# Kernel optimization log

Hardware: AMD Instinct MI355X
Metric: run time of the kernel (lower is better)

## Reference

```python
import jax, jax.numpy as jnp
import numpy as np

# alpha clamp limits: balance=False -> [exp(-1/5), exp(-1/25)]
ALPHA_MIN = float(np.exp(-1.0 / 5.0))
ALPHA_MAX = float(np.exp(-1.0 / 25.0))
T_CROP = 100


def setup_inputs() -> dict:
    key = jax.random.key(0)
    k1, k2, k3 = jax.random.split(key, 3)
    B, T, D, H = 128, 1000, 1024, 256
    x = jax.random.normal(k1, (B, T, D), dtype=jnp.float32)
    bound = float(np.sqrt(1.0 / D))
    W = jax.random.uniform(k2, (H, D), minval=-bound, maxval=bound, dtype=jnp.float32)
    alpha = jax.random.uniform(k3, (H,), minval=ALPHA_MIN, maxval=ALPHA_MAX, dtype=jnp.float32)
    return {"x": x, "W": W, "alpha": alpha}


def reference(x, W, alpha):
    # x: [B, T, D], W: [H, D], alpha: [H]
    a = jnp.clip(alpha, ALPHA_MIN, ALPHA_MAX)
    Wx = jnp.einsum('btd,hd->bth', x, W)  # [B, T, H]
    T = Wx.shape[1]
    mask = (jnp.arange(T) >= T_CROP).astype(Wx.dtype)  # [T]
    Wx_t = jnp.moveaxis(Wx, 1, 0)  # [T, B, H]

    def step(carry, inp):
        ut, out = carry
        wx, m = inp
        ut = a * ut + (1.0 - a) * wx
        out = out + m * jax.nn.softmax(ut, axis=-1)
        return (ut, out), None

    B, H = Wx.shape[0], Wx.shape[2]
    init = (jnp.zeros((B, H), Wx.dtype), jnp.zeros((B, H), Wx.dtype))
    (_, out), _ = jax.lax.scan(step, init, (Wx_t, mask))
    return out  # [B, H]
```

## Files before the change

### kernel.cpp

```cpp
#include <hip/hip_runtime.h>
#include <hip/hip_bf16.h>

#define B_    128
#define T_    1000
#define D_    1024
#define H_    256
#define TCROP 100
#define CHUNK 50
#define NCH   20
#define CSKIP (TCROP/CHUNK)

typedef __attribute__((ext_vector_type(8))) short bfrag8;
typedef __attribute__((ext_vector_type(4))) float f32x4;

__device__ __forceinline__ unsigned short f2bf(float f) {
    union { float f; unsigned int u; } v; v.f = f;
    unsigned int u = v.u;
    u += 0x7FFFu + ((u >> 16) & 1u);
    return (unsigned short)(u >> 16);
}
__device__ __forceinline__ float bf2f(unsigned short u) {
    union { unsigned int u; float f; } v; v.u = ((unsigned int)u) << 16;
    return v.f;
}

__global__ __launch_bounds__(256) void wconv_kernel(
        const float* __restrict__ W, unsigned short* __restrict__ Wbf) {
    const int i = (blockIdx.x * 256 + threadIdx.x) * 8;
    float4 f0 = *(const float4*)(W + i);
    float4 f1 = *(const float4*)(W + i + 4);
    bfrag8 v;
    v[0] = (short)f2bf(f0.x); v[1] = (short)f2bf(f0.y);
    v[2] = (short)f2bf(f0.z); v[3] = (short)f2bf(f0.w);
    v[4] = (short)f2bf(f1.x); v[5] = (short)f2bf(f1.y);
    v[6] = (short)f2bf(f1.z); v[7] = (short)f2bf(f1.w);
    *(bfrag8*)(Wbf + i) = v;
}

__global__ __launch_bounds__(512) void gemm_kernel(
        const float* __restrict__ x, const unsigned short* __restrict__ Wbf,
        unsigned short* __restrict__ Wx) {
    __shared__ unsigned short As[128 * 64];
    __shared__ unsigned short Bs[256 * 64];

    const int tid  = threadIdx.x;
    const int lane = tid & 63;
    const int wave = tid >> 6;
    const int wr   = wave >> 2;
    const int wc   = wave & 3;
    const int m0   = blockIdx.x * 128;

    f32x4 acc[4][4];
#pragma unroll
    for (int m = 0; m < 4; ++m)
#pragma unroll
        for (int n = 0; n < 4; ++n) acc[m][n] = (f32x4){0.f, 0.f, 0.f, 0.f};

    const int rr  = lane & 15;
    const int kh  = lane >> 4;
    const int ra0 = tid >> 3;
    const int ja  = tid & 7;

    for (int kt = 0; kt < D_; kt += 64) {
#pragma unroll
        for (int q = 0; q < 4; ++q) {
            const int li = q * 512 + tid;
            const int r  = li >> 3;
            const int j  = li & 7;
            const int jj = j ^ (r & 7);
            const unsigned short* src = Wbf + (size_t)r * D_ + kt + jj * 8;
            unsigned short* dst = &Bs[li * 8];
            __builtin_amdgcn_global_load_lds(
                (const __attribute__((address_space(1))) void*)src,
                (__attribute__((address_space(3))) void*)dst, 16, 0, 0);
        }
#pragma unroll
        for (int q = 0; q < 2; ++q) {
            const int r = ra0 + q * 64;
            const float* src = x + (size_t)(m0 + r) * D_ + kt + ja * 8;
            float4 f0 = *(const float4*)src;
            float4 f1 = *(const float4*)(src + 4);
            bfrag8 v;
            v[0] = (short)f2bf(f0.x); v[1] = (short)f2bf(f0.y);
            v[2] = (short)f2bf(f0.z); v[3] = (short)f2bf(f0.w);
            v[4] = (short)f2bf(f1.x); v[5] = (short)f2bf(f1.y);
            v[6] = (short)f2bf(f1.z); v[7] = (short)f2bf(f1.w);
            *(bfrag8*)&As[r * 64 + ((ja ^ (r & 7)) * 8)] = v;
        }
        __syncthreads();

#pragma unroll
        for (int kk = 0; kk < 2; ++kk) {
            const int c16 = kk * 4 + kh;
            bfrag8 af[4], bfr[4];
#pragma unroll
            for (int m = 0; m < 4; ++m) {
                const int row = wr * 64 + m * 16 + rr;
                af[m] = *(const bfrag8*)&As[row * 64 + ((c16 ^ (row & 7)) * 8)];
            }
#pragma unroll
            for (int n = 0; n < 4; ++n) {
                const int row = wc * 64 + n * 16 + rr;
                bfr[n] = *(const bfrag8*)&Bs[row * 64 + ((c16 ^ (row & 7)) * 8)];
            }
#pragma unroll
            for (int m = 0; m < 4; ++m)
#pragma unroll
                for (int n = 0; n < 4; ++n)
                    acc[m][n] = __builtin_amdgcn_mfma_f32_16x16x32_bf16(
                        af[m], bfr[n], acc[m][n], 0, 0, 0);
        }
        __syncthreads();
    }

    const int cl = lane & 15, rg = lane >> 4;
#pragma unroll
    for (int m = 0; m < 4; ++m)
#pragma unroll
        for (int n = 0; n < 4; ++n)
#pragma unroll
            for (int j = 0; j < 4; ++j) {
                const int row = m0 + wr * 64 + m * 16 + rg * 4 + j;
                const int col = wc * 64 + n * 16 + cl;
                Wx[(size_t)row * H_ + col] = f2bf(acc[m][n][j]);
            }
}

__global__ __launch_bounds__(64) void scanA_kernel(
        const unsigned short* __restrict__ Wx, const float* __restrict__ alpha,
        float* __restrict__ F) {
    const int c = blockIdx.x, b = blockIdx.y;
    const int lane = threadIdx.x;
    const int h = lane * 4;

    const float AMIN = 0.81873075307798182f, AMAX = 0.96078943915232320f;
    float4 al = *(const float4*)(alpha + h);
    float a[4]  = {fminf(fmaxf(al.x, AMIN), AMAX), fminf(fmaxf(al.y, AMIN), AMAX),
                   fminf(fmaxf(al.z, AMIN), AMAX), fminf(fmaxf(al.w, AMIN), AMAX)};
    float om[4] = {1.f - a[0], 1.f - a[1], 1.f - a[2], 1.f - a[3]};

    float ut[4] = {0.f, 0.f, 0.f, 0.f};
    const unsigned short* base = Wx + ((size_t)b * T_ + c * CHUNK) * H_ + h;
#pragma unroll 5
    for (int t = 0; t < CHUNK; ++t) {
        unsigned long long wv = *(const unsigned long long*)(base + (size_t)t * H_);
        ut[0] = a[0] * ut[0] + om[0] * bf2f((unsigned short)wv);
        ut[1] = a[1] * ut[1] + om[1] * bf2f((unsigned short)(wv >> 16));
        ut[2] = a[2] * ut[2] + om[2] * bf2f((unsigned short)(wv >> 32));
        ut[3] = a[3] * ut[3] + om[3] * bf2f((unsigned short)(wv >> 48));
    }
    float4 o; o.x = ut[0]; o.y = ut[1]; o.z = ut[2]; o.w = ut[3];
    *(float4*)(F + ((size_t)b * NCH + c) * H_ + h) = o;
}

__global__ __launch_bounds__(256) void scanB_kernel(
        const float* __restrict__ F, const float* __restrict__ alpha,
        float* __restrict__ S) {
    const int b = blockIdx.x, h = threadIdx.x;
    const float AMIN = 0.81873075307798182f, AMAX = 0.96078943915232320f;
    const float a = fminf(fmaxf(alpha[h], AMIN), AMAX);
    const float aL = powf(a, (float)CHUNK);
    float s = 0.f;
    for (int c = 0; c < NCH; ++c) {
        S[((size_t)b * NCH + c) * H_ + h] = s;
        s = aL * s + F[((size_t)b * NCH + c) * H_ + h];
    }
}

__global__ __launch_bounds__(64) void scanC_kernel(
        const unsigned short* __restrict__ Wx, const float* __restrict__ alpha,
        const float* __restrict__ S, float* __restrict__ P) {
    const int c = blockIdx.x + CSKIP;
    const int b = blockIdx.y;
    const int lane = threadIdx.x;
    const int h = lane * 4;

    const float AMIN = 0.81873075307798182f, AMAX = 0.96078943915232320f;
    float4 al = *(const float4*)(alpha + h);
    float a[4]  = {fminf(fmaxf(al.x, AMIN), AMAX), fminf(fmaxf(al.y, AMIN), AMAX),
                   fminf(fmaxf(al.z, AMIN), AMAX), fminf(fmaxf(al.w, AMIN), AMAX)};
    float om[4] = {1.f - a[0], 1.f - a[1], 1.f - a[2], 1.f - a[3]};

    float4 s0 = *(const float4*)(S + ((size_t)b * NCH + c) * H_ + h);
    float ut[4]  = {s0.x, s0.y, s0.z, s0.w};
    float acc[4] = {0.f, 0.f, 0.f, 0.f};

    const unsigned short* base = Wx + ((size_t)b * T_ + c * CHUNK) * H_ + h;
#pragma unroll 5
    for (int t = 0; t < CHUNK; ++t) {
        unsigned long long wv = *(const unsigned long long*)(base + (size_t)t * H_);
        ut[0] = a[0] * ut[0] + om[0] * bf2f((unsigned short)wv);
        ut[1] = a[1] * ut[1] + om[1] * bf2f((unsigned short)(wv >> 16));
        ut[2] = a[2] * ut[2] + om[2] * bf2f((unsigned short)(wv >> 32));
        ut[3] = a[3] * ut[3] + om[3] * bf2f((unsigned short)(wv >> 48));

        float e0 = __expf(ut[0]);
        float e1 = __expf(ut[1]);
        float e2 = __expf(ut[2]);
        float e3 = __expf(ut[3]);
        float s = (e0 + e1) + (e2 + e3);
        s += __shfl_xor(s, 1);
        s += __shfl_xor(s, 2);
        s += __shfl_xor(s, 4);
        s += __shfl_xor(s, 8);
        s += __shfl_xor(s, 16);
        s += __shfl_xor(s, 32);
        const float r = 1.0f / s;
        acc[0] += e0 * r; acc[1] += e1 * r; acc[2] += e2 * r; acc[3] += e3 * r;
    }
    float4 o; o.x = acc[0]; o.y = acc[1]; o.z = acc[2]; o.w = acc[3];
    *(float4*)(P + ((size_t)b * NCH + c) * H_ + h) = o;
}

__global__ __launch_bounds__(256) void scanD_kernel(
        const float* __restrict__ P, float* __restrict__ out) {
    const int b = blockIdx.x, h = threadIdx.x;
    float s = 0.f;
    for (int c = CSKIP; c < NCH; ++c) s += P[((size_t)b * NCH + c) * H_ + h];
    out[(size_t)b * H_ + h] = s;
}

extern "C" void kernel_launch(void* const* d_in, const int* in_sizes, int n_in,
                              void* d_out, int out_size, void* d_ws, size_t ws_size,
                              hipStream_t stream) {
    const float* x     = (const float*)d_in[0];
    const float* W     = (const float*)d_in[1];
    const float* alpha = (const float*)d_in[2];
    float* out = (float*)d_out;

    char* ws = (char*)d_ws;
    unsigned short* Wbf = (unsigned short*)ws;
    unsigned short* Wx  = (unsigned short*)(ws + (1 << 20));
    float* F = (float*)(ws + (size_t)68 * (1 << 20));
    float* S = (float*)(ws + (size_t)72 * (1 << 20));
    float* P = (float*)(ws + (size_t)76 * (1 << 20));

    wconv_kernel<<<128, 256, 0, stream>>>(W, Wbf);
    gemm_kernel<<<(B_ * T_) / 128, 512, 0, stream>>>(x, Wbf, Wx);
    scanA_kernel<<<dim3(NCH, B_), 64, 0, stream>>>(Wx, alpha, F);
    scanB_kernel<<<B_, H_, 0, stream>>>(F, alpha, S);
    scanC_kernel<<<dim3(NCH - CSKIP, B_), 64, 0, stream>>>(Wx, alpha, S, P);
    scanD_kernel<<<B_, H_, 0, stream>>>(P, out);
}
```

Before: 175.1 us.

## Double-buffer GEMM LDS tiles, shrink scan chunks, batch softmax reductions

The GEMM now double-buffers the A and B shared-memory tiles. Global loads for the next K tile are issued before the MFMA work on the current tile, so the loop needs one barrier per iteration instead of two. The scan chunk size drops from 50 to 20, giving 50 chunks, which raises the number of parallel blocks in the chunked scan kernels. scanC also batches four timesteps of wave-wide softmax-sum shuffles together to expose ILP. In exchange, the GEMM uses twice the LDS, which may lower occupancy, and the larger F/S/P intermediates need workspace offsets to be moved.

```diff
diff --git a/kernel.cpp b/kernel.cpp
--- a/kernel.cpp
+++ b/kernel.cpp
@@ -6,12 +6,13 @@
 #define D_    1024
 #define H_    256
 #define TCROP 100
-#define CHUNK 50
-#define NCH   20
-#define CSKIP (TCROP/CHUNK)
+#define CHUNK 20
+#define NCH   50
+#define CSKIP 5
 
 typedef __attribute__((ext_vector_type(8))) short bfrag8;
 typedef __attribute__((ext_vector_type(4))) float f32x4;
+typedef unsigned long long ull;
 
 __device__ __forceinline__ unsigned short f2bf(float f) {
     union { float f; unsigned int u; } v; v.f = f;
@@ -23,25 +24,28 @@
     union { unsigned int u; float f; } v; v.u = ((unsigned int)u) << 16;
     return v.f;
 }
+__device__ __forceinline__ bfrag8 cvt8(float4 f0, float4 f1) {
+    bfrag8 v;
+    v[0] = (short)f2bf(f0.x); v[1] = (short)f2bf(f0.y);
+    v[2] = (short)f2bf(f0.z); v[3] = (short)f2bf(f0.w);
+    v[4] = (short)f2bf(f1.x); v[5] = (short)f2bf(f1.y);
+    v[6] = (short)f2bf(f1.z); v[7] = (short)f2bf(f1.w);
+    return v;
+}
 
 __global__ __launch_bounds__(256) void wconv_kernel(
         const float* __restrict__ W, unsigned short* __restrict__ Wbf) {
     const int i = (blockIdx.x * 256 + threadIdx.x) * 8;
     float4 f0 = *(const float4*)(W + i);
     float4 f1 = *(const float4*)(W + i + 4);
-    bfrag8 v;
-    v[0] = (short)f2bf(f0.x); v[1] = (short)f2bf(f0.y);
-    v[2] = (short)f2bf(f0.z); v[3] = (short)f2bf(f0.w);
-    v[4] = (short)f2bf(f1.x); v[5] = (short)f2bf(f1.y);
-    v[6] = (short)f2bf(f1.z); v[7] = (short)f2bf(f1.w);
-    *(bfrag8*)(Wbf + i) = v;
+    *(bfrag8*)(Wbf + i) = cvt8(f0, f1);
 }
 
 __global__ __launch_bounds__(512) void gemm_kernel(
         const float* __restrict__ x, const unsigned short* __restrict__ Wbf,
         unsigned short* __restrict__ Wx) {
-    __shared__ unsigned short As[128 * 64];
-    __shared__ unsigned short Bs[256 * 64];
+    __shared__ unsigned short As[2][128 * 64];
+    __shared__ unsigned short Bs[2][256 * 64];
 
     const int tid  = threadIdx.x;
     const int lane = tid & 63;
@@ -60,35 +64,52 @@
     const int kh  = lane >> 4;
     const int ra0 = tid >> 3;
     const int ja  = tid & 7;
-
-    for (int kt = 0; kt < D_; kt += 64) {
-#pragma unroll
-        for (int q = 0; q < 4; ++q) {
-            const int li = q * 512 + tid;
-            const int r  = li >> 3;
-            const int j  = li & 7;
-            const int jj = j ^ (r & 7);
-            const unsigned short* src = Wbf + (size_t)r * D_ + kt + jj * 8;
-            unsigned short* dst = &Bs[li * 8];
-            __builtin_amdgcn_global_load_lds(
-                (const __attribute__((address_space(1))) void*)src,
-                (__attribute__((address_space(3))) void*)dst, 16, 0, 0);
-        }
-#pragma unroll
-        for (int q = 0; q < 2; ++q) {
-            const int r = ra0 + q * 64;
-            const float* src = x + (size_t)(m0 + r) * D_ + kt + ja * 8;
-            float4 f0 = *(const float4*)src;
-            float4 f1 = *(const float4*)(src + 4);
-            bfrag8 v;
-            v[0] = (short)f2bf(f0.x); v[1] = (short)f2bf(f0.y);
-            v[2] = (short)f2bf(f0.z); v[3] = (short)f2bf(f0.w);
-            v[4] = (short)f2bf(f1.x); v[5] = (short)f2bf(f1.y);
-            v[6] = (short)f2bf(f1.z); v[7] = (short)f2bf(f1.w);
-            *(bfrag8*)&As[r * 64 + ((ja ^ (r & 7)) * 8)] = v;
-        }
-        __syncthreads();
-
+    const int sa  = (ja ^ (ra0 & 7)) * 8;
+    const float* ap0 = x + (size_t)(m0 + ra0) * D_ + ja * 8;
+    const float* ap1 = ap0 + (size_t)64 * D_;
+
+#pragma unroll
+    for (int q = 0; q < 4; ++q) {
+        const int li = q * 512 + tid;
+        const int r = li >> 3, j = li & 7;
+        const int jj = j ^ (r & 7);
+        __builtin_amdgcn_global_load_lds(
+            (const __attribute__((address_space(1))) void*)(Wbf + (size_t)r * D_ + jj * 8),
+            (__attribute__((address_space(3))) void*)&Bs[0][li * 8], 16, 0, 0);
+    }
+    {
+        float4 f00 = *(const float4*)ap0;
+        float4 f01 = *(const float4*)(ap0 + 4);
+        float4 f10 = *(const float4*)ap1;
+        float4 f11 = *(const float4*)(ap1 + 4);
+        *(bfrag8*)&As[0][ra0 * 64 + sa]        = cvt8(f00, f01);
+        *(bfrag8*)&As[0][(ra0 + 64) * 64 + sa] = cvt8(f10, f11);
+    }
+    asm volatile("s_waitcnt vmcnt(0) lgkmcnt(0)" ::: "memory");
+    __builtin_amdgcn_sched_barrier(0);
+    __builtin_amdgcn_s_barrier();
+
+    for (int it = 0; it < 16; ++it) {
+        const int cur = it & 1, nxt = cur ^ 1;
+        float4 f00, f01, f10, f11;
+        if (it < 15) {
+            const int ktn = (it + 1) * 64;
+            f00 = *(const float4*)(ap0 + ktn);
+            f01 = *(const float4*)(ap0 + ktn + 4);
+            f10 = *(const float4*)(ap1 + ktn);
+            f11 = *(const float4*)(ap1 + ktn + 4);
+#pragma unroll
+            for (int q = 0; q < 4; ++q) {
+                const int li = q * 512 + tid;
+                const int r = li >> 3, j = li & 7;
+                const int jj = j ^ (r & 7);
+                __builtin_amdgcn_global_load_lds(
+                    (const __attribute__((address_space(1))) void*)
+                        (Wbf + (size_t)r * D_ + ktn + jj * 8),
+                    (__attribute__((address_space(3))) void*)&Bs[nxt][li * 8], 16, 0, 0);
+            }
+        }
+        __builtin_amdgcn_sched_barrier(0);
 #pragma unroll
         for (int kk = 0; kk < 2; ++kk) {
             const int c16 = kk * 4 + kh;
@@ -96,12 +117,12 @@
 #pragma unroll
             for (int m = 0; m < 4; ++m) {
                 const int row = wr * 64 + m * 16 + rr;
-                af[m] = *(const bfrag8*)&As[row * 64 + ((c16 ^ (row & 7)) * 8)];
+                af[m] = *(const bfrag8*)&As[cur][row * 64 + ((c16 ^ (row & 7)) * 8)];
             }
 #pragma unroll
             for (int n = 0; n < 4; ++n) {
                 const int row = wc * 64 + n * 16 + rr;
-                bfr[n] = *(const bfrag8*)&Bs[row * 64 + ((c16 ^ (row & 7)) * 8)];
+                bfr[n] = *(const bfrag8*)&Bs[cur][row * 64 + ((c16 ^ (row & 7)) * 8)];
             }
 #pragma unroll
             for (int m = 0; m < 4; ++m)
@@ -110,7 +131,13 @@
                     acc[m][n] = __builtin_amdgcn_mfma_f32_16x16x32_bf16(
                         af[m], bfr[n], acc[m][n], 0, 0, 0);
         }
-        __syncthreads();
+        if (it < 15) {
+            *(bfrag8*)&As[nxt][ra0 * 64 + sa]        = cvt8(f00, f01);
+            *(bfrag8*)&As[nxt][(ra0 + 64) * 64 + sa] = cvt8(f10, f11);
+        }
+        asm volatile("s_waitcnt vmcnt(0) lgkmcnt(0)" ::: "memory");
+        __builtin_amdgcn_sched_barrier(0);
+        __builtin_amdgcn_s_barrier();
     }
 
     const int cl = lane & 15, rg = lane >> 4;
@@ -141,9 +168,9 @@
 
     float ut[4] = {0.f, 0.f, 0.f, 0.f};
     const unsigned short* base = Wx + ((size_t)b * T_ + c * CHUNK) * H_ + h;
-#pragma unroll 5
+#pragma unroll 4
     for (int t = 0; t < CHUNK; ++t) {
-        unsigned long long wv = *(const unsigned long long*)(base + (size_t)t * H_);
+        ull wv = *(const ull*)(base + (size_t)t * H_);
         ut[0] = a[0] * ut[0] + om[0] * bf2f((unsigned short)wv);
         ut[1] = a[1] * ut[1] + om[1] * bf2f((unsigned short)(wv >> 16));
         ut[2] = a[2] * ut[2] + om[2] * bf2f((unsigned short)(wv >> 32));
@@ -182,33 +209,43 @@
     float om[4] = {1.f - a[0], 1.f - a[1], 1.f - a[2], 1.f - a[3]};
 
     float4 s0 = *(const float4*)(S + ((size_t)b * NCH + c) * H_ + h);
-    float ut[4]  = {s0.x, s0.y, s0.z, s0.w};
-    float acc[4] = {0.f, 0.f, 0.f, 0.f};
+    float ut[4]   = {s0.x, s0.y, s0.z, s0.w};
+    float acc4[4] = {0.f, 0.f, 0.f, 0.f};
 
     const unsigned short* base = Wx + ((size_t)b * T_ + c * CHUNK) * H_ + h;
-#pragma unroll 5
-    for (int t = 0; t < CHUNK; ++t) {
-        unsigned long long wv = *(const unsigned long long*)(base + (size_t)t * H_);
-        ut[0] = a[0] * ut[0] + om[0] * bf2f((unsigned short)wv);
-        ut[1] = a[1] * ut[1] + om[1] * bf2f((unsigned short)(wv >> 16));
-        ut[2] = a[2] * ut[2] + om[2] * bf2f((unsigned short)(wv >> 32));
-        ut[3] = a[3] * ut[3] + om[3] * bf2f((unsigned short)(wv >> 48));
-
-        float e0 = __expf(ut[0]);
-        float e1 = __expf(ut[1]);
-        float e2 = __expf(ut[2]);
-        float e3 = __expf(ut[3]);
-        float s = (e0 + e1) + (e2 + e3);
-        s += __shfl_xor(s, 1);
-        s += __shfl_xor(s, 2);
-        s += __shfl_xor(s, 4);
-        s += __shfl_xor(s, 8);
-        s += __shfl_xor(s, 16);
-        s += __shfl_xor(s, 32);
-        const float r = 1.0f / s;
-        acc[0] += e0 * r; acc[1] += e1 * r; acc[2] += e2 * r; acc[3] += e3 * r;
-    }
-    float4 o; o.x = acc[0]; o.y = acc[1]; o.z = acc[2]; o.w = acc[3];
+#pragma unroll
+    for (int tb = 0; tb < CHUNK; tb += 4) {
+        float e[4][4], sl[4];
+#pragma unroll
+        for (int q = 0; q < 4; ++q) {
+            ull wv = *(const ull*)(base + (size_t)(tb + q) * H_);
+            ut[0] = a[0] * ut[0] + om[0] * bf2f((unsigned short)wv);
+            ut[1] = a[1] * ut[1] + om[1] * bf2f((unsigned short)(wv >> 16));
+            ut[2] = a[2] * ut[2] + om[2] * bf2f((unsigned short)(wv >> 32));
+            ut[3] = a[3] * ut[3] + om[3] * bf2f((unsigned short)(wv >> 48));
+            e[q][0] = __expf(ut[0]);
+            e[q][1] = __expf(ut[1]);
+            e[q][2] = __expf(ut[2]);
+            e[q][3] = __expf(ut[3]);
+            sl[q] = (e[q][0] + e[q][1]) + (e[q][2] + e[q][3]);
+        }
+#pragma unroll
+        for (int d = 1; d < 64; d <<= 1) {
+            sl[0] += __shfl_xor(sl[0], d);
+            sl[1] += __shfl_xor(sl[1], d);
+            sl[2] += __shfl_xor(sl[2], d);
+            sl[3] += __shfl_xor(sl[3], d);
+        }
+#pragma unroll
+        for (int q = 0; q < 4; ++q) {
+            const float rcp = 1.0f / sl[q];
+            acc4[0] += e[q][0] * rcp;
+            acc4[1] += e[q][1] * rcp;
+            acc4[2] += e[q][2] * rcp;
+            acc4[3] += e[q][3] * rcp;
+        }
+    }
+    float4 o; o.x = acc4[0]; o.y = acc4[1]; o.z = acc4[2]; o.w = acc4[3];
     *(float4*)(P + ((size_t)b * NCH + c) * H_ + h) = o;
 }
 
@@ -230,10 +267,10 @@
 
     char* ws = (char*)d_ws;
     unsigned short* Wbf = (unsigned short*)ws;
-    unsigned short* Wx  = (unsigned short*)(ws + (1 << 20));
-    float* F = (float*)(ws + (size_t)68 * (1 << 20));
-    float* S = (float*)(ws + (size_t)72 * (1 << 20));
-    float* P = (float*)(ws + (size_t)76 * (1 << 20));
+    unsigned short* Wx  = (unsigned short*)(ws + ((size_t)1 << 20));
+    float* F = (float*)(ws + ((size_t)70 << 20));
+    float* S = (float*)(ws + ((size_t)80 << 20));
+    float* P = (float*)(ws + ((size_t)90 << 20));
 
     wconv_kernel<<<128, 256, 0, stream>>>(W, Wbf);
     gemm_kernel<<<(B_ * T_) / 128, 512, 0, stream>>>(x, Wbf, Wx);
```

Result: slower. 209.6 us (+19.7%).
